# Optimization experiments

Hardware: AMD Instinct MI355X
Metric: run time of the kernel (lower is better)

## Reference

```python
import jax, jax.numpy as jnp
import numpy as np
from math import sqrt

BLOCK = 64  # block_size from init_kwargs


def setup_inputs() -> dict:
    key = jax.random.key(0)
    kq, kk, kv = jax.random.split(key, 3)
    b, t, e = 16, 8192, 64
    return {
        "Q": jax.random.normal(kq, (b, t, e), dtype=jnp.float32),
        "K": jax.random.normal(kk, (b, t, e), dtype=jnp.float32),
        "V": jax.random.normal(kv, (b, t, e), dtype=jnp.float32),
    }


def reference(Q, K, V):
    b, t, e = Q.shape
    # strided column indices: last position of every block
    cols = jnp.arange(BLOCK - 1, t, BLOCK)            # [n_cols] = [t // BLOCK]
    # scores of every query against the gathered key columns
    Z = jnp.einsum('bte,bce->btc', Q, K[:, cols]) / sqrt(e)  # [b, t, n_cols]
    # causal mask: query at position i may not attend to a column j > i
    causal = jnp.arange(t)[:, None] < cols[None, :]   # [t, n_cols], True = masked
    Z = jnp.where(causal, -jnp.inf, Z)
    # rows before the first column (i < BLOCK-1) are fully masked -> keep zeros
    A = jnp.zeros_like(Z).at[:, BLOCK - 1:].set(
        jax.nn.softmax(Z[:, BLOCK - 1:], axis=-1))
    out = jnp.einsum('btc,bce->bte', A, V[:, cols])   # [b, t, e]
    return out, A
```

## Files before the change

### kernel.cpp

```cpp
#include <hip/hip_runtime.h>
#include <math.h>


#define TSEQ 8192
#define EDIM 64
#define NCOL 128
#define NBATCH 16

typedef __attribute__((ext_vector_type(8))) short short8;
typedef __attribute__((ext_vector_type(4))) float f32x4;

__device__ __forceinline__ unsigned short f2bf(float f) {
    unsigned int u = __float_as_uint(f);
    return (unsigned short)((u + 0x7fffu + ((u >> 16) & 1u)) >> 16);
}
__device__ __forceinline__ float bf2f(unsigned short h) {
    return __uint_as_float(((unsigned int)h) << 16);
}

__global__ __launch_bounds__(256, 3)
void cba_kernel(const float* __restrict__ Q,
                const float* __restrict__ K,
                const float* __restrict__ V,
                float* __restrict__ Out,
                float* __restrict__ A)
{
    __shared__ unsigned short Kc[NCOL][72];
    __shared__ unsigned short VcT[EDIM][136];
    __shared__ unsigned short Aw[64][136];

    const int tid  = threadIdx.x;
    const int lane = tid & 63;
    const int wid  = tid >> 6;
    const int b    = blockIdx.x >> 7;
    const int m    = blockIdx.x & 127;

    const size_t rowbase = (size_t)b * TSEQ + ((size_t)m << 6);

    {
        const int j = tid >> 1;
        const int h = (tid & 1) << 5;
        const size_t src = ((size_t)b * TSEQ + (j * 64 + 63)) * EDIM + h;
        const float4* ks = (const float4*)(K + src);
        const float4* vs = (const float4*)(V + src);
        #pragma unroll
        for (int t = 0; t < 8; ++t) {
            float4 kf = ks[t];
            unsigned int p0 = (unsigned int)f2bf(kf.x) | ((unsigned int)f2bf(kf.y) << 16);
            unsigned int p1 = (unsigned int)f2bf(kf.z) | ((unsigned int)f2bf(kf.w) << 16);
            *(unsigned int*)&Kc[j][h + 4 * t]     = p0;
            *(unsigned int*)&Kc[j][h + 4 * t + 2] = p1;
        }
        #pragma unroll
        for (int t = 0; t < 8; ++t) {
            float4 vf = vs[t];
            VcT[h + 4 * t + 0][j] = f2bf(vf.x);
            VcT[h + 4 * t + 1][j] = f2bf(vf.y);
            VcT[h + 4 * t + 2][j] = f2bf(vf.z);
            VcT[h + 4 * t + 3][j] = f2bf(vf.w);
        }
    }

    const int kq = (lane >> 4) << 3;
    short8 qa[2];
    {
        const int qrow = (wid << 4) + (lane & 15);
        const float* qp = Q + (rowbase + qrow) * EDIM;
        #pragma unroll
        for (int s = 0; s < 2; ++s) {
            float4 f0 = *(const float4*)(qp + 32 * s + kq);
            float4 f1 = *(const float4*)(qp + 32 * s + kq + 4);
            short8 v;
            v[0] = (short)f2bf(f0.x * 0.125f); v[1] = (short)f2bf(f0.y * 0.125f);
            v[2] = (short)f2bf(f0.z * 0.125f); v[3] = (short)f2bf(f0.w * 0.125f);
            v[4] = (short)f2bf(f1.x * 0.125f); v[5] = (short)f2bf(f1.y * 0.125f);
            v[6] = (short)f2bf(f1.z * 0.125f); v[7] = (short)f2bf(f1.w * 0.125f);
            qa[s] = v;
        }
    }
    __syncthreads();

    f32x4 acc[8];
    #pragma unroll
    for (int t = 0; t < 8; ++t) acc[t] = (f32x4)0.f;
    #pragma unroll
    for (int t = 0; t < 8; ++t) {
        const unsigned short* kr = &Kc[(t << 4) + (lane & 15)][0];
        short8 b0 = *(const short8*)(kr + kq);
        short8 b1 = *(const short8*)(kr + 32 + kq);
        acc[t] = __builtin_amdgcn_mfma_f32_16x16x32_bf16(qa[0], b0, acc[t], 0, 0, 0);
        acc[t] = __builtin_amdgcn_mfma_f32_16x16x32_bf16(qa[1], b1, acc[t], 0, 0, 0);
    }

    const int rb = (wid << 4) + ((lane >> 4) << 2);
    float rinv[4];
    #pragma unroll
    for (int reg = 0; reg < 4; ++reg) {
        const int r  = rb + reg;
        const int nv = m + (r == 63 ? 1 : 0);
        float sum = 0.f;
        #pragma unroll
        for (int t = 0; t < 8; ++t) {
            const int jc = (t << 4) + (lane & 15);
            float e = (jc < nv) ? __expf(acc[t][reg]) : 0.f;
            acc[t][reg] = e;
            sum += e;
        }
        sum += __shfl_xor(sum, 1); sum += __shfl_xor(sum, 2);
        sum += __shfl_xor(sum, 4); sum += __shfl_xor(sum, 8);
        rinv[reg] = (sum > 0.f) ? 1.0f / sum : 0.f;
    }

    #pragma unroll
    for (int reg = 0; reg < 4; ++reg) {
        #pragma unroll
        for (int t = 0; t < 8; ++t)
            Aw[rb + reg][(t << 4) + (lane & 15)] = f2bf(acc[t][reg] * rinv[reg]);
    }
    __syncthreads();

    {
        const int row = tid >> 2;
        const int c0  = (tid & 3) << 5;
        const unsigned short* src = &Aw[row][c0];
        float4* dst = (float4*)(A + (rowbase + row) * NCOL + c0);
        #pragma unroll
        for (int g = 0; g < 4; ++g) {
            short8 u = *(const short8*)(src + 8 * g);
            float4 lo, hi;
            lo.x = bf2f((unsigned short)u[0]); lo.y = bf2f((unsigned short)u[1]);
            lo.z = bf2f((unsigned short)u[2]); lo.w = bf2f((unsigned short)u[3]);
            hi.x = bf2f((unsigned short)u[4]); hi.y = bf2f((unsigned short)u[5]);
            hi.z = bf2f((unsigned short)u[6]); hi.w = bf2f((unsigned short)u[7]);
            dst[2 * g] = lo; dst[2 * g + 1] = hi;
        }
    }

    short8 af[4];
    {
        const unsigned short* ar = &Aw[(wid << 4) + (lane & 15)][0];
        #pragma unroll
        for (int s = 0; s < 4; ++s) af[s] = *(const short8*)(ar + (s << 5) + kq);
    }
    f32x4 oacc[4];
    #pragma unroll
    for (int t = 0; t < 4; ++t) oacc[t] = (f32x4)0.f;
    #pragma unroll
    for (int t = 0; t < 4; ++t) {
        const unsigned short* vr = &VcT[(t << 4) + (lane & 15)][0];
        #pragma unroll
        for (int s = 0; s < 4; ++s) {
            short8 vb = *(const short8*)(vr + (s << 5) + kq);
            oacc[t] = __builtin_amdgcn_mfma_f32_16x16x32_bf16(af[s], vb, oacc[t], 0, 0, 0);
        }
    }
    #pragma unroll
    for (int t = 0; t < 4; ++t) {
        #pragma unroll
        for (int reg = 0; reg < 4; ++reg) {
            Out[(rowbase + rb + reg) * EDIM + (t << 4) + (lane & 15)] = oacc[t][reg];
        }
    }
}

extern "C" void kernel_launch(void* const* d_in, const int* in_sizes, int n_in,
                              void* d_out, int out_size, void* d_ws, size_t ws_size,
                              hipStream_t stream) {
    const float* Q = (const float*)d_in[0];
    const float* K = (const float*)d_in[1];
    const float* V = (const float*)d_in[2];
    float* Out = (float*)d_out;
    float* A   = Out + (size_t)NBATCH * TSEQ * EDIM;

    cba_kernel<<<dim3(NBATCH * NCOL), dim3(256), 0, stream>>>(Q, K, V, Out, A);
}
```

Measured before the change: 188.6 us.

## Process four query tiles per block reusing staged K/V columns and prefetch Q

Each block now handles four consecutive 64-row query tiles, so the gathered K and V columns are loaded and converted to bf16 once per four tiles instead of once per tile. The next tile's Q rows are prefetched into registers while the current tile's scores are computed. A is now written to global memory straight from the fp32 accumulators instead of being round-tripped through bf16 shared memory, which changes its precision. The grid shrinks to 512 blocks with launch bounds lowered to 2 waves per SIMD, so fewer blocks are available to fill the GPU.

```diff
diff --git a/kernel.cpp b/kernel.cpp
--- a/kernel.cpp
+++ b/kernel.cpp
@@ -6,6 +6,7 @@
 #define EDIM 64
 #define NCOL 128
 #define NBATCH 16
+#define MPG 4
 
 typedef __attribute__((ext_vector_type(8))) short short8;
 typedef __attribute__((ext_vector_type(4))) float f32x4;
@@ -14,11 +15,8 @@
     unsigned int u = __float_as_uint(f);
     return (unsigned short)((u + 0x7fffu + ((u >> 16) & 1u)) >> 16);
 }
-__device__ __forceinline__ float bf2f(unsigned short h) {
-    return __uint_as_float(((unsigned int)h) << 16);
-}
 
-__global__ __launch_bounds__(256, 3)
+__global__ __launch_bounds__(256, 2)
 void cba_kernel(const float* __restrict__ Q,
                 const float* __restrict__ K,
                 const float* __restrict__ V,
@@ -32,10 +30,23 @@
     const int tid  = threadIdx.x;
     const int lane = tid & 63;
     const int wid  = tid >> 6;
-    const int b    = blockIdx.x >> 7;
-    const int m    = blockIdx.x & 127;
+    const int b    = blockIdx.x >> 5;
+    const int mg   = blockIdx.x & 31;
 
-    const size_t rowbase = (size_t)b * TSEQ + ((size_t)m << 6);
+    const int c   = lane & 15;
+    const int kq  = (lane >> 4) << 3;
+    const int rb  = (wid << 4) + ((lane >> 4) << 2);
+    const int qr  = (wid << 4) + c;
+
+    float4 qf[4];
+    {
+        const int m0 = mg * MPG;
+        const float* qp = Q + ((size_t)b * TSEQ + (m0 << 6) + qr) * EDIM;
+        qf[0] = *(const float4*)(qp + kq);
+        qf[1] = *(const float4*)(qp + kq + 4);
+        qf[2] = *(const float4*)(qp + 32 + kq);
+        qf[3] = *(const float4*)(qp + 32 + kq + 4);
+    }
 
     {
         const int j = tid >> 1;
@@ -60,16 +71,16 @@
             VcT[h + 4 * t + 3][j] = f2bf(vf.w);
         }
     }
+    __syncthreads();
 
-    const int kq = (lane >> 4) << 3;
-    short8 qa[2];
-    {
-        const int qrow = (wid << 4) + (lane & 15);
-        const float* qp = Q + (rowbase + qrow) * EDIM;
+    for (int it = 0; it < MPG; ++it) {
+        const int m = mg * MPG + it;
+        const size_t rowbase = (size_t)b * TSEQ + ((size_t)m << 6);
+
+        short8 qa[2];
         #pragma unroll
         for (int s = 0; s < 2; ++s) {
-            float4 f0 = *(const float4*)(qp + 32 * s + kq);
-            float4 f1 = *(const float4*)(qp + 32 * s + kq + 4);
+            float4 f0 = qf[2 * s], f1 = qf[2 * s + 1];
             short8 v;
             v[0] = (short)f2bf(f0.x * 0.125f); v[1] = (short)f2bf(f0.y * 0.125f);
             v[2] = (short)f2bf(f0.z * 0.125f); v[3] = (short)f2bf(f0.w * 0.125f);
@@ -77,88 +88,87 @@
             v[6] = (short)f2bf(f1.z * 0.125f); v[7] = (short)f2bf(f1.w * 0.125f);
             qa[s] = v;
         }
-    }
-    __syncthreads();
 
-    f32x4 acc[8];
-    #pragma unroll
-    for (int t = 0; t < 8; ++t) acc[t] = (f32x4)0.f;
-    #pragma unroll
-    for (int t = 0; t < 8; ++t) {
-        const unsigned short* kr = &Kc[(t << 4) + (lane & 15)][0];
-        short8 b0 = *(const short8*)(kr + kq);
-        short8 b1 = *(const short8*)(kr + 32 + kq);
-        acc[t] = __builtin_amdgcn_mfma_f32_16x16x32_bf16(qa[0], b0, acc[t], 0, 0, 0);
-        acc[t] = __builtin_amdgcn_mfma_f32_16x16x32_bf16(qa[1], b1, acc[t], 0, 0, 0);
-    }
-
-    const int rb = (wid << 4) + ((lane >> 4) << 2);
-    float rinv[4];
-    #pragma unroll
-    for (int reg = 0; reg < 4; ++reg) {
-        const int r  = rb + reg;
-        const int nv = m + (r == 63 ? 1 : 0);
-        float sum = 0.f;
+        f32x4 acc[8];
+        #pragma unroll
+        for (int t = 0; t < 8; ++t) acc[t] = (f32x4)0.f;
         #pragma unroll
         for (int t = 0; t < 8; ++t) {
-            const int jc = (t << 4) + (lane & 15);
-            float e = (jc < nv) ? __expf(acc[t][reg]) : 0.f;
-            acc[t][reg] = e;
-            sum += e;
+            const unsigned short* kr = &Kc[(t << 4) + c][0];
+            short8 b0 = *(const short8*)(kr + kq);
+            short8 b1 = *(const short8*)(kr + 32 + kq);
+            acc[t] = __builtin_amdgcn_mfma_f32_16x16x32_bf16(qa[0], b0, acc[t], 0, 0, 0);
+            acc[t] = __builtin_amdgcn_mfma_f32_16x16x32_bf16(qa[1], b1, acc[t], 0, 0, 0);
         }
-        sum += __shfl_xor(sum, 1); sum += __shfl_xor(sum, 2);
-        sum += __shfl_xor(sum, 4); sum += __shfl_xor(sum, 8);
-        rinv[reg] = (sum > 0.f) ? 1.0f / sum : 0.f;
-    }
 
-    #pragma unroll
-    for (int reg = 0; reg < 4; ++reg) {
-        #pragma unroll
-        for (int t = 0; t < 8; ++t)
-            Aw[rb + reg][(t << 4) + (lane & 15)] = f2bf(acc[t][reg] * rinv[reg]);
-    }
-    __syncthreads();
+        if (it + 1 < MPG) {
+            const float* qp = Q + (rowbase + 64 + qr) * EDIM;
+            qf[0] = *(const float4*)(qp + kq);
+            qf[1] = *(const float4*)(qp + kq + 4);
+            qf[2] = *(const float4*)(qp + 32 + kq);
+            qf[3] = *(const float4*)(qp + 32 + kq + 4);
+        }
 
-    {
-        const int row = tid >> 2;
-        const int c0  = (tid & 3) << 5;
-        const unsigned short* src = &Aw[row][c0];
-        float4* dst = (float4*)(A + (rowbase + row) * NCOL + c0);
-        #pragma unroll
-        for (int g = 0; g < 4; ++g) {
-            short8 u = *(const short8*)(src + 8 * g);
-            float4 lo, hi;
-            lo.x = bf2f((unsigned short)u[0]); lo.y = bf2f((unsigned short)u[1]);
-            lo.z = bf2f((unsigned short)u[2]); lo.w = bf2f((unsigned short)u[3]);
-            hi.x = bf2f((unsigned short)u[4]); hi.y = bf2f((unsigned short)u[5]);
-            hi.z = bf2f((unsigned short)u[6]); hi.w = bf2f((unsigned short)u[7]);
-            dst[2 * g] = lo; dst[2 * g + 1] = hi;
-        }
-    }
-
-    short8 af[4];
-    {
-        const unsigned short* ar = &Aw[(wid << 4) + (lane & 15)][0];
-        #pragma unroll
-        for (int s = 0; s < 4; ++s) af[s] = *(const short8*)(ar + (s << 5) + kq);
-    }
-    f32x4 oacc[4];
-    #pragma unroll
-    for (int t = 0; t < 4; ++t) oacc[t] = (f32x4)0.f;
-    #pragma unroll
-    for (int t = 0; t < 4; ++t) {
-        const unsigned short* vr = &VcT[(t << 4) + (lane & 15)][0];
-        #pragma unroll
-        for (int s = 0; s < 4; ++s) {
-            short8 vb = *(const short8*)(vr + (s << 5) + kq);
-            oacc[t] = __builtin_amdgcn_mfma_f32_16x16x32_bf16(af[s], vb, oacc[t], 0, 0, 0);
-        }
-    }
-    #pragma unroll
-    for (int t = 0; t < 4; ++t) {
         #pragma unroll
         for (int reg = 0; reg < 4; ++reg) {
-            Out[(rowbase + rb + reg) * EDIM + (t << 4) + (lane & 15)] = oacc[t][reg];
+            const int r  = rb + reg;
+            const int nv = m + (r == 63 ? 1 : 0);
+            float sum = 0.f;
+            #pragma unroll
+            for (int t = 0; t < 8; ++t) {
+                const int jc = (t << 4) + c;
+                float e = (jc < nv) ? __expf(acc[t][reg]) : 0.f;
+                acc[t][reg] = e;
+                sum += e;
+            }
+            sum += __shfl_xor(sum, 1); sum += __shfl_xor(sum, 2);
+            sum += __shfl_xor(sum, 4); sum += __shfl_xor(sum, 8);
+            const float rinv = (sum > 0.f) ? 1.0f / sum : 0.f;
+            #pragma unroll
+            for (int t = 0; t < 8; ++t) acc[t][reg] *= rinv;
+        }
+
+        #pragma unroll
+        for (int reg = 0; reg < 4; ++reg) {
+            float* ap = A + (rowbase + rb + reg) * NCOL + c;
+            #pragma unroll
+            for (int t = 0; t < 8; ++t) ap[t << 4] = acc[t][reg];
+        }
+
+        __syncthreads();
+
+        #pragma unroll
+        for (int reg = 0; reg < 4; ++reg) {
+            #pragma unroll
+            for (int t = 0; t < 8; ++t)
+                Aw[rb + reg][(t << 4) + c] = f2bf(acc[t][reg]);
+        }
+        __syncthreads();
+
+        short8 af[4];
+        {
+            const unsigned short* ar = &Aw[qr][0];
+            #pragma unroll
+            for (int s = 0; s < 4; ++s) af[s] = *(const short8*)(ar + (s << 5) + kq);
+        }
+        f32x4 oacc[4];
+        #pragma unroll
+        for (int t = 0; t < 4; ++t) oacc[t] = (f32x4)0.f;
+        #pragma unroll
+        for (int t = 0; t < 4; ++t) {
+            const unsigned short* vr = &VcT[(t << 4) + c][0];
+            #pragma unroll
+            for (int s = 0; s < 4; ++s) {
+                short8 vb = *(const short8*)(vr + (s << 5) + kq);
+                oacc[t] = __builtin_amdgcn_mfma_f32_16x16x32_bf16(af[s], vb, oacc[t], 0, 0, 0);
+            }
+        }
+
+        #pragma unroll
+        for (int t = 0; t < 4; ++t) {
+            #pragma unroll
+            for (int reg = 0; reg < 4; ++reg)
+                Out[(rowbase + rb + reg) * EDIM + (t << 4) + c] = oacc[t][reg];
         }
     }
 }
@@ -172,5 +182,5 @@
     float* Out = (float*)d_out;
     float* A   = Out + (size_t)NBATCH * TSEQ * EDIM;
 
-    cba_kernel<<<dim3(NBATCH * NCOL), dim3(256), 0, stream>>>(Q, K, V, Out, A);
+    cba_kernel<<<dim3(NBATCH * 32), dim3(256), 0, stream>>>(Q, K, V, Out, A);
 }
```

Result: faster. 172.4 us (-8.6%).
